# Optimization experiments

Hardware: AMD Instinct MI355X
Metric: run time of the kernel (lower is better)

Reference implementation:

```python
import jax, jax.numpy as jnp
import numpy as np

NUM_ATOMS = 50000
NUM_EDGES = 200000  # even: edges come in (fwd, rev) pairs
D_V, D_E, D_H = 133, 14, 256
DEPTH = 3


def setup_inputs() -> dict:
    key = jax.random.key(0)
    ks = jax.random.split(key, 12)
    half = NUM_EDGES // 2
    src = jax.random.randint(ks[0], (half,), 0, NUM_ATOMS)
    dst = jax.random.randint(ks[1], (half,), 0, NUM_ATOMS)
    v = jnp.concatenate([src, dst])
    w = jnp.concatenate([dst, src])
    edge_index = jnp.stack([v, w])  # [2, E]
    rev_edge_index = jnp.concatenate([jnp.arange(half) + half, jnp.arange(half)])

    def lin(k, out_d, in_d):
        return jax.random.normal(k, (out_d, in_d), jnp.float32) / np.sqrt(in_d)

    return {
        "V": jax.random.normal(ks[2], (NUM_ATOMS, D_V), jnp.float32),
        "E_feat": jax.random.normal(ks[3], (NUM_EDGES, D_E), jnp.float32),
        "edge_index": edge_index,
        "rev_edge_index": rev_edge_index,
        "Wi_atom": lin(ks[4], D_H, D_V),
        "Wi_bond": lin(ks[5], D_H, D_V + D_E),
        "Wh_atom": lin(ks[6], D_H, D_H),
        "Wh_bond": lin(ks[7], D_H, D_H),
        "Wf_atom": lin(ks[8], D_H, D_H),
        "Wf_bond": lin(ks[9], D_H, D_H),
        "Wo_atom": lin(ks[10], D_H, D_V + D_H),
    }


def _sum_and_max_into_atoms(H_e, w_idx, num_atoms):
    a_sum = jax.ops.segment_sum(H_e, w_idx, num_segments=num_atoms)
    a_max = jax.ops.segment_max(H_e, w_idx, num_segments=num_atoms)
    a_max = jnp.where(jnp.isfinite(a_max), a_max, 0.0)  # empty segments -> 0
    return a_sum, a_max


def _fuse(H, m, Wf):
    # Fusion(kind='mlp', residual=True), dropout=0:
    # residual update with a small MLP on the combined signal
    return H + jax.nn.relu((H + m) @ Wf.T)


def reference(V, E_feat, edge_index, rev_edge_index, Wi_atom, Wi_bond,
              Wh_atom, Wh_bond, Wf_atom, Wf_bond, Wo_atom):
    tau = jax.nn.relu
    num_atoms = V.shape[0]
    v = edge_index[0]
    w = edge_index[1]

    H_a = tau(V @ Wi_atom.T)                                        # [N, d_h]
    H_b = tau(jnp.concatenate([V[v], E_feat], axis=1) @ Wi_bond.T)  # [E, d_h]

    for _ in range(1, DEPTH):
        a_sum, a_max = _sum_and_max_into_atoms(H_b, w, num_atoms)
        gate = a_sum * a_max
        m_a = gate @ Wh_atom.T
        H_a = _fuse(H_a, m_a, Wf_atom)

        M_b = a_sum[v] - H_b[rev_edge_index]
        m_b = M_b @ Wh_bond.T
        H_b = _fuse(H_b, m_b, Wf_bond)

    a_sum, _ = _sum_and_max_into_atoms(H_b, w, num_atoms)
    H_atom = tau(jnp.concatenate([V, a_sum], axis=1) @ Wo_atom.T)   # [N, d_h]
    return H_atom
```

## Files before the change

kernel.cpp:

```cpp
#include <hip/hip_runtime.h>
#include <hip/hip_bf16.h>

#define NATOM 50000
#define NEDGE 200000
#define HALF  100000
#define DV    133
#define DE    14
#define DH    256
#define KVP   160
#define NBLK_SCAN ((NATOM + 255) / 256)

typedef __bf16  bf16x8 __attribute__((ext_vector_type(8)));
typedef __bf16  bf16x4 __attribute__((ext_vector_type(4)));
typedef float   f32x4  __attribute__((ext_vector_type(4)));

enum { EPI_RELU = 0, EPI_ADDBASE = 1, EPI_FUSE = 2, EPI_NONE = 3, EPI_RELUADD = 4 };
enum { AM_PLAIN = 0, AM_GATE = 1, AM_GDIFF = 2, AM_VF32 = 3, AM_XB = 4, AM_F32 = 5 };

__device__ __forceinline__ void gll16(const void* g, void* l) {
    __builtin_amdgcn_global_load_lds(
        (const __attribute__((address_space(1))) unsigned int*)g,
        (__attribute__((address_space(3))) unsigned int*)l, 16, 0, 0);
}
__device__ __forceinline__ void drain_barrier() {
    __builtin_amdgcn_s_waitcnt(0);
    __syncthreads();
}

struct GArgs {
    const __bf16* A; int lda;
    const float* asumf; const __bf16* amaxb;
    const __bf16* HbG; const int* vidx; const int* rev;
    const float* Vf; const float* Ef;
    const __bf16* W; int ldw;
    const __bf16* base; __bf16* C; float* Cf;
    int Mloc; int part0; int off0; int off1;
};

template<int AMODE, int EPI, int CLOC, int STF32, int KITERS>
__global__ __launch_bounds__(512, 2) void gemmk(GArgs g, int nblk) {
    __shared__ __bf16 Alds[4096];
    __shared__ __bf16 Blds[8192];
    const int tid  = threadIdx.x;
    const int lane = tid & 63, wv = tid >> 6;
    const int quad = lane >> 4, l16 = lane & 15;
    const int wr = (wv >> 2) * 64, wc = (wv & 3) * 64;
    const int lrow = lane >> 2, lu = lane & 3;

    for (int blk = blockIdx.x; blk < nblk; blk += gridDim.x) {
        const int gr0 = blk * 128;

        const int rs = tid >> 2, seg = tid & 3;
        const float *sp = nullptr; const __bf16 *hp = nullptr, *mp = nullptr;
        const float *vp = nullptr, *ep = nullptr;
        if (AMODE != AM_PLAIN) {
            int grs = gr0 + rs; if (grs > g.Mloc - 1) grs = g.Mloc - 1;
            const int maps = (grs < g.part0) ? g.off0 + grs : g.off1 + grs - g.part0;
            if (AMODE == AM_GATE)  { sp = g.asumf + (size_t)maps * DH; mp = g.amaxb + (size_t)maps * DH; }
            if (AMODE == AM_GDIFF) { sp = g.asumf + (size_t)g.vidx[maps] * DH; hp = g.HbG + (size_t)g.rev[maps] * DH; }
            if (AMODE == AM_F32)   { sp = g.asumf + (size_t)maps * DH; }
            if (AMODE == AM_VF32)  { vp = g.Vf + (size_t)maps * DV; }
            if (AMODE == AM_XB)    { vp = g.Vf + (size_t)g.vidx[maps] * DV; ep = g.Ef + (size_t)maps * DE; }
        }

        f32x4 acc[16];
#pragma unroll
        for (int i = 0; i < 16; ++i) acc[i] = (f32x4){0.f, 0.f, 0.f, 0.f};

        for (int kk = 0; kk < KITERS; ++kk) {
#pragma unroll
            for (int s = 0; s < 2; ++s) {
                int cl = (wv * 2 + s) * 16 + lrow;
                gll16(g.W + (size_t)cl * g.ldw + kk * 32 + lu * 8,
                      Blds + (wv * 2 + s) * 512);
            }
            if (AMODE == AM_PLAIN) {
                int r = wv * 16 + lrow;
                int gra = gr0 + r; if (gra > g.Mloc - 1) gra = g.Mloc - 1;
                gll16(g.A + (size_t)gra * g.lda + kk * 32 + lu * 8,
                      Alds + wv * 512);
            } else {
                bf16x8 o0;
                const int cb = kk * 32 + seg * 8;
                if (AMODE == AM_GATE || AMODE == AM_GDIFF || AMODE == AM_F32) {
                    f32x4 s0 = *(const f32x4*)(sp + cb);
                    f32x4 s1 = *(const f32x4*)(sp + cb + 4);
                    if (AMODE == AM_GATE) {
                        bf16x8 m0 = *(const bf16x8*)(mp + cb);
#pragma unroll
                        for (int j = 0; j < 4; ++j) {
                            o0[j]     = (__bf16)(s0[j] * (float)m0[j]);
                            o0[4 + j] = (__bf16)(s1[j] * (float)m0[4 + j]);
                        }
                    } else if (AMODE == AM_GDIFF) {
                        bf16x8 h0 = *(const bf16x8*)(hp + cb);
#pragma unroll
                        for (int j = 0; j < 4; ++j) {
                            o0[j]     = (__bf16)(s0[j] - (float)h0[j]);
                            o0[4 + j] = (__bf16)(s1[j] - (float)h0[4 + j]);
                        }
                    } else {
#pragma unroll
                        for (int j = 0; j < 4; ++j) {
                            o0[j]     = (__bf16)s0[j];
                            o0[4 + j] = (__bf16)s1[j];
                        }
                    }
                } else {
                    if (kk < 4) {
                        f32x4 x0, x1;
                        __builtin_memcpy(&x0, vp + cb, 16);
                        __builtin_memcpy(&x1, vp + cb + 4, 16);
#pragma unroll
                        for (int j = 0; j < 4; ++j) {
                            o0[j] = (__bf16)x0[j]; o0[4 + j] = (__bf16)x1[j];
                        }
                    } else {
#pragma unroll
                        for (int j = 0; j < 8; ++j) {
                            int c0 = cb + j;
                            float y0 = 0.f;
                            if (c0 < DV) y0 = vp[c0];
                            else if (AMODE == AM_XB && c0 < DV + DE) y0 = ep[c0 - DV];
                            o0[j] = (__bf16)y0;
                        }
                    }
                }
                *(bf16x8*)(Alds + rs * 32 + seg * 8) = o0;
            }
            drain_barrier();

            bf16x8 af[4], bfv[4];
#pragma unroll
            for (int m = 0; m < 4; ++m)
                af[m] = *(const bf16x8*)(Alds + (wr + m * 16 + l16) * 32 + quad * 8);
#pragma unroll
            for (int n = 0; n < 4; ++n)
                bfv[n] = *(const bf16x8*)(Blds + (wc + n * 16 + l16) * 32 + quad * 8);
#pragma unroll
            for (int m = 0; m < 4; ++m)
#pragma unroll
                for (int n = 0; n < 4; ++n)
                    acc[m * 4 + n] = __builtin_amdgcn_mfma_f32_16x16x32_bf16(
                        af[m], bfv[n], acc[m * 4 + n], 0, 0, 0);
            drain_barrier();
        }

#pragma unroll
        for (int m = 0; m < 4; ++m)
#pragma unroll
        for (int n = 0; n < 4; ++n)
#pragma unroll
        for (int r = 0; r < 4; ++r) {
            int gr = gr0 + wr + m * 16 + quad * 4 + r;
            if (gr < g.Mloc) {
                int mapped = (gr < g.part0) ? g.off0 + gr : g.off1 + gr - g.part0;
                int crow = CLOC ? gr : mapped;
                int col = wc + n * 16 + l16;
                size_t co = (size_t)crow * DH + col;
                float v = acc[m * 4 + n][r];
                float res;
                if (EPI == EPI_RELU)       res = v > 0.f ? v : 0.f;
                else if (EPI == EPI_NONE)  res = v;
                else {
                    float b = (float)g.base[(size_t)mapped * DH + col];
                    if (EPI == EPI_ADDBASE)      res = b + v;
                    else if (EPI == EPI_FUSE)    res = b + (v > 0.f ? v : 0.f);
                    else        { res = b + v; res = res > 0.f ? res : 0.f; }
                }
                if (STF32) g.Cf[co] = res;
                else       g.C[co]  = (__bf16)res;
            }
        }
    }
}

__global__ void count_deg(const int* __restrict__ widx, int* __restrict__ cnt) {
    int e = blockIdx.x * 256 + threadIdx.x;
    if (e < NEDGE) atomicAdd(&cnt[widx[e]], 1);
}

__global__ __launch_bounds__(256) void scan_p1(const int* __restrict__ cnt,
                                               int* __restrict__ rowptr,
                                               int* __restrict__ bsum) {
    __shared__ int sm[256];
    const int tid = threadIdx.x;
    const int i = blockIdx.x * 256 + tid;
    int v = (i < NATOM) ? cnt[i] : 0;
    sm[tid] = v;
    __syncthreads();
    for (int off = 1; off < 256; off <<= 1) {
        int t = (tid >= off) ? sm[tid - off] : 0;
        __syncthreads();
        sm[tid] += t;
        __syncthreads();
    }
    if (i < NATOM) rowptr[i] = sm[tid] - v;
    if (tid == 255) bsum[blockIdx.x] = sm[255];
}

__global__ __launch_bounds__(256) void scan_p2(int* __restrict__ bsum) {
    __shared__ int sm[256];
    const int tid = threadIdx.x;
    int v = (tid < NBLK_SCAN) ? bsum[tid] : 0;
    sm[tid] = v;
    __syncthreads();
    for (int off = 1; off < 256; off <<= 1) {
        int t = (tid >= off) ? sm[tid - off] : 0;
        __syncthreads();
        sm[tid] += t;
        __syncthreads();
    }
    if (tid < NBLK_SCAN) bsum[tid] = sm[tid] - v;
    if (tid == 255) bsum[NBLK_SCAN] = sm[255];
}

__global__ __launch_bounds__(256) void scan_p3(int* __restrict__ rowptr,
                                               int* __restrict__ cursor,
                                               const int* __restrict__ bsum) {
    const int i = blockIdx.x * 256 + threadIdx.x;
    if (i < NATOM) {
        int r = rowptr[i] + bsum[blockIdx.x];
        rowptr[i] = r;
        cursor[i] = r;
    }
    if (i == 0) rowptr[NATOM] = bsum[NBLK_SCAN];
}

__global__ void fill_csr(const int* __restrict__ widx, int* __restrict__ cursor,
                         int* __restrict__ eid) {
    int e = blockIdx.x * 256 + threadIdx.x;
    if (e >= NEDGE) return;
    int pos = atomicAdd(&cursor[widx[e]], 1);
    eid[pos] = e;
}

template<int WITHMAX>
__global__ __launch_bounds__(256) void seg_reduce(
    const __bf16* __restrict__ Hb, const int* __restrict__ rowptr,
    const int* __restrict__ eid,
    float* __restrict__ asum, __bf16* __restrict__ amaxb)
{
    int a = blockIdx.x * 4 + (threadIdx.x >> 6);
    if (a >= NATOM) return;
    const int lane = threadIdx.x & 63;
    const int beg = rowptr[a], end = rowptr[a + 1];
    float s0 = 0.f, s1 = 0.f, s2 = 0.f, s3 = 0.f;
    float m0 = 0.f, m1 = 0.f, m2 = 0.f, m3 = 0.f;
    for (int i = beg; i < end; ++i) {
        int e = eid[i];
        bf16x4 h = *(const bf16x4*)(Hb + (size_t)e * DH + lane * 4);
        float v0 = (float)h[0], v1 = (float)h[1], v2 = (float)h[2], v3 = (float)h[3];
        s0 += v0; s1 += v1; s2 += v2; s3 += v3;
        if (WITHMAX) {
            m0 = fmaxf(m0, v0); m1 = fmaxf(m1, v1);
            m2 = fmaxf(m2, v2); m3 = fmaxf(m3, v3);
        }
    }
    size_t o = (size_t)a * DH + lane * 4;
    *(f32x4*)(asum + o) = (f32x4){s0, s1, s2, s3};
    if (WITHMAX) {
        bf16x4 mv; mv[0] = (__bf16)m0; mv[1] = (__bf16)m1; mv[2] = (__bf16)m2; mv[3] = (__bf16)m3;
        *(bf16x4*)(amaxb + o) = mv;
    }
}

__global__ void pad_w2(const float* __restrict__ src, __bf16* __restrict__ dst,
                       int srcld, int coloff, int KS, int KD) {
    int i = blockIdx.x * 256 + threadIdx.x;
    if (i >= 256 * KD) return;
    int n = i / KD, c = i - n * KD;
    dst[i] = (c < KS) ? (__bf16)src[(size_t)n * srcld + coloff + c] : (__bf16)0.f;
}

static inline int cdiv(long a, long b) { return (int)((a + b - 1) / b); }
static inline int gsz2(int nblk) { return nblk < 2048 ? nblk : 2048; }

extern "C" void kernel_launch(void* const* d_in, const int* in_sizes, int n_in,
                              void* d_out, int out_size, void* d_ws, size_t ws_size,
                              hipStream_t stream) {
    const float* V    = (const float*)d_in[0];
    const float* Ef   = (const float*)d_in[1];
    const int*   ei   = (const int*)d_in[2];
    const int*   rev  = (const int*)d_in[3];
    const float* Wi_a = (const float*)d_in[4];
    const float* Wi_b = (const float*)d_in[5];
    const float* Wh_a = (const float*)d_in[6];
    const float* Wh_b = (const float*)d_in[7];
    const float* Wf_a = (const float*)d_in[8];
    const float* Wf_b = (const float*)d_in[9];
    const float* Wo   = (const float*)d_in[10];
    float* out = (float*)d_out;

    const int* vidx = ei;
    const int* widx = ei + NEDGE;

    char* ws = (char*)d_ws;
    __bf16* Hb    = (__bf16*)(ws + 0);
    __bf16* Ha    = (__bf16*)(ws + 102400000);
    char*   S     = ws + 128000000;
    float*  asum  = (float*)(ws + 192000000);
    __bf16* amaxb = (__bf16*)(S + 0);
    __bf16* Ta    = (__bf16*)(S + 25600000);
    __bf16* Tb    = (__bf16*)(S + 0);
    __bf16* T     = (__bf16*)(S + 25600000);
    __bf16* Wia   = (__bf16*)(ws + 243200000);
    __bf16* Wib   = (__bf16*)(ws + 243281920);
    __bf16* Wo1   = (__bf16*)(ws + 243363840);
    __bf16* Wo2   = (__bf16*)(ws + 243445760);
    __bf16* Wha   = (__bf16*)(ws + 243576832);
    __bf16* Whb   = (__bf16*)(ws + 243707904);
    __bf16* Wfa   = (__bf16*)(ws + 243838976);
    __bf16* Wfb   = (__bf16*)(ws + 243970048);
    int*  rowptr  = (int*)(ws + 244101120);
    int*  cursor  = (int*)(ws + 244301312);
    int*  eid     = (int*)(ws + 244501504);
    int*  bsum    = (int*)(ws + 128000000);
    (void)ws_size;

    hipMemsetAsync(cursor, 0, NATOM * sizeof(int), stream);
    count_deg<<<cdiv(NEDGE, 256), 256, 0, stream>>>(widx, cursor);
    scan_p1<<<NBLK_SCAN, 256, 0, stream>>>(cursor, rowptr, bsum);
    scan_p2<<<1, 256, 0, stream>>>(bsum);
    scan_p3<<<NBLK_SCAN, 256, 0, stream>>>(rowptr, cursor, bsum);
    fill_csr<<<cdiv(NEDGE, 256), 256, 0, stream>>>(widx, cursor, eid);

    pad_w2<<<cdiv(256 * KVP, 256), 256, 0, stream>>>(Wi_a, Wia, DV, 0, DV, KVP);
    pad_w2<<<cdiv(256 * KVP, 256), 256, 0, stream>>>(Wi_b, Wib, DV + DE, 0, DV + DE, KVP);
    pad_w2<<<cdiv(256 * KVP, 256), 256, 0, stream>>>(Wo, Wo1, DV + DH, 0, DV, KVP);
    pad_w2<<<cdiv(256 * DH, 256), 256, 0, stream>>>(Wo, Wo2, DV + DH, DV, DH, DH);
    pad_w2<<<cdiv(256 * DH, 256), 256, 0, stream>>>(Wh_a, Wha, DH, 0, DH, DH);
    pad_w2<<<cdiv(256 * DH, 256), 256, 0, stream>>>(Wh_b, Whb, DH, 0, DH, DH);
    pad_w2<<<cdiv(256 * DH, 256), 256, 0, stream>>>(Wf_a, Wfa, DH, 0, DH, DH);
    pad_w2<<<cdiv(256 * DH, 256), 256, 0, stream>>>(Wf_b, Wfb, DH, 0, DH, DH);

    GArgs ga{};
    ga.asumf = asum; ga.amaxb = amaxb; ga.HbG = Hb; ga.vidx = vidx; ga.rev = rev;
    ga.Vf = V; ga.Ef = Ef;

    {
        int nblk = cdiv(NATOM, 128);
        ga.W = Wia; ga.ldw = KVP; ga.C = Ha;
        ga.Mloc = NATOM; ga.part0 = NATOM; ga.off0 = 0; ga.off1 = 0;
        gemmk<AM_VF32, EPI_RELU, 0, 0, 5><<<gsz2(nblk), 512, 0, stream>>>(ga, nblk);
    }
    {
        int nblk = cdiv(NEDGE, 128);
        ga.W = Wib; ga.ldw = KVP; ga.C = Hb;
        ga.Mloc = NEDGE; ga.part0 = NEDGE; ga.off0 = 0; ga.off1 = 0;
        gemmk<AM_XB, EPI_RELU, 0, 0, 5><<<gsz2(nblk), 512, 0, stream>>>(ga, nblk);
    }

    for (int it = 0; it < 2; ++it) {
        seg_reduce<1><<<cdiv(NATOM, 4), 256, 0, stream>>>(Hb, rowptr, eid, asum, amaxb);

        {
            int nblk = cdiv(NATOM, 128);
            ga.W = Wha; ga.ldw = DH; ga.base = Ha; ga.C = Ta;
            ga.Mloc = NATOM; ga.part0 = NATOM; ga.off0 = 0; ga.off1 = 0;
            gemmk<AM_GATE, EPI_ADDBASE, 1, 0, 8><<<gsz2(nblk), 512, 0, stream>>>(ga, nblk);
            ga.A = Ta; ga.lda = DH; ga.W = Wfa; ga.base = Ha; ga.C = Ha;
            gemmk<AM_PLAIN, EPI_FUSE, 0, 0, 8><<<gsz2(nblk), 512, 0, stream>>>(ga, nblk);
        }

        for (int c = 0; c < 2; ++c) {
            int nblk = cdiv(HALF, 128);
            ga.W = Whb; ga.ldw = DH; ga.base = Hb; ga.C = Tb;
            ga.Mloc = HALF; ga.part0 = HALF / 2; ga.off0 = c * 50000; ga.off1 = HALF + c * 50000;
            gemmk<AM_GDIFF, EPI_ADDBASE, 1, 0, 8><<<gsz2(nblk), 512, 0, stream>>>(ga, nblk);
            ga.A = Tb; ga.lda = DH; ga.W = Wfb; ga.base = Hb; ga.C = Hb;
            gemmk<AM_PLAIN, EPI_FUSE, 0, 0, 8><<<gsz2(nblk), 512, 0, stream>>>(ga, nblk);
        }
    }

    seg_reduce<0><<<cdiv(NATOM, 4), 256, 0, stream>>>(Hb, rowptr, eid, asum, nullptr);
    {
        int nblk = cdiv(NATOM, 128);
        ga.Mloc = NATOM; ga.part0 = NATOM; ga.off0 = 0; ga.off1 = 0;
        ga.W = Wo1; ga.ldw = KVP; ga.C = T;
        gemmk<AM_VF32, EPI_NONE, 0, 0, 5><<<gsz2(nblk), 512, 0, stream>>>(ga, nblk);
        ga.W = Wo2; ga.ldw = DH; ga.base = T; ga.Cf = out;
        gemmk<AM_F32, EPI_RELUADD, 0, 1, 8><<<gsz2(nblk), 512, 0, stream>>>(ga, nblk);
    }
}
```

Measured before the change: 1.204 ms.

## Preload full A tile into LDS and double-buffer W tiles in GEMM

The GEMM used to load one 32-wide K slice of A and W per iteration, with two full barriers each time. Now all K slices of the gathered or converted A rows are staged into LDS in one pass before any compute. W tiles are double-buffered, and the next slice is prefetched while MFMAs run on the current one. This aims to raise memory-level parallelism and hide global load latency behind compute. The cost is much larger LDS use: 96KB for K=256, which likely stops two 512-thread blocks from sharing a CU and so lowers occupancy.

```diff
diff --git a/kernel.cpp b/kernel.cpp
--- a/kernel.cpp
+++ b/kernel.cpp
@@ -39,8 +39,8 @@
 
 template<int AMODE, int EPI, int CLOC, int STF32, int KITERS>
 __global__ __launch_bounds__(512, 2) void gemmk(GArgs g, int nblk) {
-    __shared__ __bf16 Alds[4096];
-    __shared__ __bf16 Blds[8192];
+    __shared__ __align__(16) __bf16 Alds[KITERS * 4096];
+    __shared__ __align__(16) __bf16 Blds[2 * 8192];
     const int tid  = threadIdx.x;
     const int lane = tid & 63, wv = tid >> 6;
     const int quad = lane >> 4, l16 = lane & 15;
@@ -63,23 +63,20 @@
             if (AMODE == AM_XB)    { vp = g.Vf + (size_t)g.vidx[maps] * DV; ep = g.Ef + (size_t)maps * DE; }
         }
 
-        f32x4 acc[16];
-#pragma unroll
-        for (int i = 0; i < 16; ++i) acc[i] = (f32x4){0.f, 0.f, 0.f, 0.f};
-
-        for (int kk = 0; kk < KITERS; ++kk) {
-#pragma unroll
-            for (int s = 0; s < 2; ++s) {
-                int cl = (wv * 2 + s) * 16 + lrow;
-                gll16(g.W + (size_t)cl * g.ldw + kk * 32 + lu * 8,
-                      Blds + (wv * 2 + s) * 512);
-            }
-            if (AMODE == AM_PLAIN) {
-                int r = wv * 16 + lrow;
-                int gra = gr0 + r; if (gra > g.Mloc - 1) gra = g.Mloc - 1;
+#pragma unroll
+        for (int s = 0; s < 2; ++s) {
+            int cl = (wv * 2 + s) * 16 + lrow;
+            gll16(g.W + (size_t)cl * g.ldw + lu * 8, Blds + (wv * 2 + s) * 512);
+        }
+        if (AMODE == AM_PLAIN) {
+            int gra = gr0 + wv * 16 + lrow; if (gra > g.Mloc - 1) gra = g.Mloc - 1;
+#pragma unroll
+            for (int kk = 0; kk < KITERS; ++kk)
                 gll16(g.A + (size_t)gra * g.lda + kk * 32 + lu * 8,
-                      Alds + wv * 512);
-            } else {
+                      Alds + kk * 4096 + wv * 512);
+        } else {
+#pragma unroll
+            for (int kk = 0; kk < KITERS; ++kk) {
                 bf16x8 o0;
                 const int cb = kk * 32 + seg * 8;
                 if (AMODE == AM_GATE || AMODE == AM_GDIFF || AMODE == AM_F32) {
@@ -126,17 +123,33 @@
                         }
                     }
                 }
-                *(bf16x8*)(Alds + rs * 32 + seg * 8) = o0;
+                *(bf16x8*)(Alds + kk * 4096 + rs * 32 + seg * 8) = o0;
             }
-            drain_barrier();
-
+        }
+        drain_barrier();
+
+        f32x4 acc[16];
+#pragma unroll
+        for (int i = 0; i < 16; ++i) acc[i] = (f32x4){0.f, 0.f, 0.f, 0.f};
+
+        for (int k = 0; k < KITERS; ++k) {
+            if (k + 1 < KITERS) {
+#pragma unroll
+                for (int s = 0; s < 2; ++s) {
+                    int cl = (wv * 2 + s) * 16 + lrow;
+                    gll16(g.W + (size_t)cl * g.ldw + (k + 1) * 32 + lu * 8,
+                          Blds + ((k + 1) & 1) * 8192 + (wv * 2 + s) * 512);
+                }
+            }
+            const __bf16* Ak = Alds + k * 4096;
+            const __bf16* Bb = Blds + (k & 1) * 8192;
             bf16x8 af[4], bfv[4];
 #pragma unroll
             for (int m = 0; m < 4; ++m)
-                af[m] = *(const bf16x8*)(Alds + (wr + m * 16 + l16) * 32 + quad * 8);
+                af[m] = *(const bf16x8*)(Ak + (wr + m * 16 + l16) * 32 + quad * 8);
 #pragma unroll
             for (int n = 0; n < 4; ++n)
-                bfv[n] = *(const bf16x8*)(Blds + (wc + n * 16 + l16) * 32 + quad * 8);
+                bfv[n] = *(const bf16x8*)(Bb + (wc + n * 16 + l16) * 32 + quad * 8);
 #pragma unroll
             for (int m = 0; m < 4; ++m)
 #pragma unroll
```

Result: slower. 1.326 ms (+10.1%).

## Fuse chained message/fusion GEMMs via LDS and load operands directly to registers

Applied to the files above, without the earlier changes.

Replaces the generic LDS-staged GEMM with two kernels. One is a direct-to-register GEMM for the input and output projections; the final Wo projection now runs as a single K-concatenated pass instead of two launches through an intermediate buffer. The other is a fused two-GEMM kernel that keeps the Wh result in swizzled LDS and feeds it straight into the Wf GEMM with the residual ReLU epilogue. For bonds, each block processes forward and reverse edge pairs together so that H_b[rev] is read from rows the same block updates, and a bf16 copy of a_sum is emitted for this path. This removes intermediate global round trips, extra launches and barriers, at the cost of uncoalesced per-lane global operand loads, repeated weight reads from cache, and slightly lower precision in the bond message.

```diff
diff --git a/kernel.cpp b/kernel.cpp
--- a/kernel.cpp
+++ b/kernel.cpp
@@ -14,163 +14,251 @@
 typedef __bf16  bf16x4 __attribute__((ext_vector_type(4)));
 typedef float   f32x4  __attribute__((ext_vector_type(4)));
 
-enum { EPI_RELU = 0, EPI_ADDBASE = 1, EPI_FUSE = 2, EPI_NONE = 3, EPI_RELUADD = 4 };
-enum { AM_PLAIN = 0, AM_GATE = 1, AM_GDIFF = 2, AM_VF32 = 3, AM_XB = 4, AM_F32 = 5 };
-
-__device__ __forceinline__ void gll16(const void* g, void* l) {
-    __builtin_amdgcn_global_load_lds(
-        (const __attribute__((address_space(1))) unsigned int*)g,
-        (__attribute__((address_space(3))) unsigned int*)l, 16, 0, 0);
-}
 __device__ __forceinline__ void drain_barrier() {
     __builtin_amdgcn_s_waitcnt(0);
     __syncthreads();
 }
 
-struct GArgs {
-    const __bf16* A; int lda;
-    const float* asumf; const __bf16* amaxb;
-    const __bf16* HbG; const int* vidx; const int* rev;
-    const float* Vf; const float* Ef;
-    const __bf16* W; int ldw;
-    const __bf16* base; __bf16* C; float* Cf;
-    int Mloc; int part0; int off0; int off1;
+
+struct DArgs {
+    const float* Vf; const float* Ef; const float* asumf;
+    const int* vidx;
+    const __bf16* W1; const __bf16* W2;
+    __bf16* C; float* Cf;
+    int M;
 };
 
-template<int AMODE, int EPI, int CLOC, int STF32, int KITERS>
-__global__ __launch_bounds__(512, 2) void gemmk(GArgs g, int nblk) {
-    __shared__ __bf16 Alds[4096];
-    __shared__ __bf16 Blds[8192];
-    const int tid  = threadIdx.x;
+template<int MODE, int KITERS>
+__global__ __launch_bounds__(512, 4) void dgemm(DArgs g) {
+    const int tid = threadIdx.x;
     const int lane = tid & 63, wv = tid >> 6;
     const int quad = lane >> 4, l16 = lane & 15;
     const int wr = (wv >> 2) * 64, wc = (wv & 3) * 64;
-    const int lrow = lane >> 2, lu = lane & 3;
-
-    for (int blk = blockIdx.x; blk < nblk; blk += gridDim.x) {
-        const int gr0 = blk * 128;
-
-        const int rs = tid >> 2, seg = tid & 3;
-        const float *sp = nullptr; const __bf16 *hp = nullptr, *mp = nullptr;
-        const float *vp = nullptr, *ep = nullptr;
-        if (AMODE != AM_PLAIN) {
-            int grs = gr0 + rs; if (grs > g.Mloc - 1) grs = g.Mloc - 1;
-            const int maps = (grs < g.part0) ? g.off0 + grs : g.off1 + grs - g.part0;
-            if (AMODE == AM_GATE)  { sp = g.asumf + (size_t)maps * DH; mp = g.amaxb + (size_t)maps * DH; }
-            if (AMODE == AM_GDIFF) { sp = g.asumf + (size_t)g.vidx[maps] * DH; hp = g.HbG + (size_t)g.rev[maps] * DH; }
-            if (AMODE == AM_F32)   { sp = g.asumf + (size_t)maps * DH; }
-            if (AMODE == AM_VF32)  { vp = g.Vf + (size_t)maps * DV; }
-            if (AMODE == AM_XB)    { vp = g.Vf + (size_t)g.vidx[maps] * DV; ep = g.Ef + (size_t)maps * DE; }
-        }
-
-        f32x4 acc[16];
-#pragma unroll
-        for (int i = 0; i < 16; ++i) acc[i] = (f32x4){0.f, 0.f, 0.f, 0.f};
-
-        for (int kk = 0; kk < KITERS; ++kk) {
-#pragma unroll
-            for (int s = 0; s < 2; ++s) {
-                int cl = (wv * 2 + s) * 16 + lrow;
-                gll16(g.W + (size_t)cl * g.ldw + kk * 32 + lu * 8,
-                      Blds + (wv * 2 + s) * 512);
-            }
-            if (AMODE == AM_PLAIN) {
-                int r = wv * 16 + lrow;
-                int gra = gr0 + r; if (gra > g.Mloc - 1) gra = g.Mloc - 1;
-                gll16(g.A + (size_t)gra * g.lda + kk * 32 + lu * 8,
-                      Alds + wv * 512);
-            } else {
-                bf16x8 o0;
-                const int cb = kk * 32 + seg * 8;
-                if (AMODE == AM_GATE || AMODE == AM_GDIFF || AMODE == AM_F32) {
-                    f32x4 s0 = *(const f32x4*)(sp + cb);
-                    f32x4 s1 = *(const f32x4*)(sp + cb + 4);
-                    if (AMODE == AM_GATE) {
-                        bf16x8 m0 = *(const bf16x8*)(mp + cb);
-#pragma unroll
-                        for (int j = 0; j < 4; ++j) {
-                            o0[j]     = (__bf16)(s0[j] * (float)m0[j]);
-                            o0[4 + j] = (__bf16)(s1[j] * (float)m0[4 + j]);
-                        }
-                    } else if (AMODE == AM_GDIFF) {
-                        bf16x8 h0 = *(const bf16x8*)(hp + cb);
-#pragma unroll
-                        for (int j = 0; j < 4; ++j) {
-                            o0[j]     = (__bf16)(s0[j] - (float)h0[j]);
-                            o0[4 + j] = (__bf16)(s1[j] - (float)h0[4 + j]);
-                        }
-                    } else {
-#pragma unroll
-                        for (int j = 0; j < 4; ++j) {
-                            o0[j]     = (__bf16)s0[j];
-                            o0[4 + j] = (__bf16)s1[j];
-                        }
+    const int gr0 = blockIdx.x * 128;
+
+    int vrow[4]; const float* epp[4];
+#pragma unroll
+    for (int m = 0; m < 4; ++m) {
+        int r = gr0 + wr + m * 16 + l16;
+        if (r > g.M - 1) r = g.M - 1;
+        vrow[m] = (MODE == 1) ? g.vidx[r] : r;
+        epp[m] = (MODE == 1) ? (g.Ef + (size_t)r * DE) : nullptr;
+    }
+
+    f32x4 acc[16];
+#pragma unroll
+    for (int i = 0; i < 16; ++i) acc[i] = (f32x4){0.f, 0.f, 0.f, 0.f};
+
+#pragma unroll
+    for (int kk = 0; kk < KITERS; ++kk) {
+        bf16x8 af[4];
+#pragma unroll
+        for (int m = 0; m < 4; ++m) {
+            const int cb = kk * 32 + quad * 8;
+            if (MODE != 2 || kk < 5) {
+                const float* vp = g.Vf + (size_t)vrow[m] * DV;
+                if (kk < 4) {
+                    f32x4 x0, x1;
+                    __builtin_memcpy(&x0, vp + cb, 16);
+                    __builtin_memcpy(&x1, vp + cb + 4, 16);
+#pragma unroll
+                    for (int j = 0; j < 4; ++j) {
+                        af[m][j] = (__bf16)x0[j]; af[m][4 + j] = (__bf16)x1[j];
                     }
                 } else {
-                    if (kk < 4) {
-                        f32x4 x0, x1;
-                        __builtin_memcpy(&x0, vp + cb, 16);
-                        __builtin_memcpy(&x1, vp + cb + 4, 16);
-#pragma unroll
-                        for (int j = 0; j < 4; ++j) {
-                            o0[j] = (__bf16)x0[j]; o0[4 + j] = (__bf16)x1[j];
-                        }
-                    } else {
-#pragma unroll
-                        for (int j = 0; j < 8; ++j) {
-                            int c0 = cb + j;
-                            float y0 = 0.f;
-                            if (c0 < DV) y0 = vp[c0];
-                            else if (AMODE == AM_XB && c0 < DV + DE) y0 = ep[c0 - DV];
-                            o0[j] = (__bf16)y0;
-                        }
+#pragma unroll
+                    for (int j = 0; j < 8; ++j) {
+                        int c = cb + j; float y = 0.f;
+                        if (c < DV) y = vp[c];
+                        else if (MODE == 1 && c < DV + DE) y = epp[m][c - DV];
+                        af[m][j] = (__bf16)y;
                     }
                 }
-                *(bf16x8*)(Alds + rs * 32 + seg * 8) = o0;
+            } else {
+                const float* sp = g.asumf + (size_t)vrow[m] * DH + (kk - 5) * 32 + quad * 8;
+                f32x4 s0 = *(const f32x4*)sp, s1 = *(const f32x4*)(sp + 4);
+#pragma unroll
+                for (int j = 0; j < 4; ++j) {
+                    af[m][j] = (__bf16)s0[j]; af[m][4 + j] = (__bf16)s1[j];
+                }
             }
-            drain_barrier();
-
-            bf16x8 af[4], bfv[4];
-#pragma unroll
-            for (int m = 0; m < 4; ++m)
-                af[m] = *(const bf16x8*)(Alds + (wr + m * 16 + l16) * 32 + quad * 8);
+        }
+        bf16x8 bfv[4];
+#pragma unroll
+        for (int n = 0; n < 4; ++n) {
+            int col = wc + n * 16 + l16;
+            const __bf16* wp;
+            if (MODE == 2 && kk >= 5) wp = g.W2 + (size_t)col * DH  + (kk - 5) * 32 + quad * 8;
+            else                      wp = g.W1 + (size_t)col * KVP + kk * 32 + quad * 8;
+            bfv[n] = *(const bf16x8*)wp;
+        }
+#pragma unroll
+        for (int m = 0; m < 4; ++m)
 #pragma unroll
             for (int n = 0; n < 4; ++n)
-                bfv[n] = *(const bf16x8*)(Blds + (wc + n * 16 + l16) * 32 + quad * 8);
-#pragma unroll
-            for (int m = 0; m < 4; ++m)
-#pragma unroll
-                for (int n = 0; n < 4; ++n)
-                    acc[m * 4 + n] = __builtin_amdgcn_mfma_f32_16x16x32_bf16(
-                        af[m], bfv[n], acc[m * 4 + n], 0, 0, 0);
-            drain_barrier();
-        }
-
+                acc[m * 4 + n] = __builtin_amdgcn_mfma_f32_16x16x32_bf16(
+                    af[m], bfv[n], acc[m * 4 + n], 0, 0, 0);
+    }
+
+#pragma unroll
+    for (int m = 0; m < 4; ++m)
+#pragma unroll
+    for (int n = 0; n < 4; ++n)
+#pragma unroll
+    for (int r = 0; r < 4; ++r) {
+        int gr = gr0 + wr + m * 16 + quad * 4 + r;
+        if (gr < g.M) {
+            int col = wc + n * 16 + l16;
+            float v = acc[m * 4 + n][r];
+            v = v > 0.f ? v : 0.f;
+            if (MODE == 2) g.Cf[(size_t)gr * DH + col] = v;
+            else           g.C [(size_t)gr * DH + col] = (__bf16)v;
+        }
+    }
+}
+
+struct FArgs {
+    const float* asumf; const __bf16* asumb; const __bf16* amaxb;
+    const int* vidx;
+    const __bf16* W1; const __bf16* W2;
+    __bf16* H;
+    int M;
+};
+
+__device__ __forceinline__ int tswz(int row, int byteInRow) {
+    return ((row << 9) + byteInRow) ^ ((row & 7) << 4);
+}
+
+template<int BOND>
+__global__ __launch_bounds__(512, 4) void fgemm(FArgs g) {
+    __shared__ __bf16 Tlds[32768];
+    const int tid = threadIdx.x;
+    const int lane = tid & 63, wv = tid >> 6;
+    const int quad = lane >> 4, l16 = lane & 15;
+    const int wr = (wv >> 2) * 64, wc = (wv & 3) * 64;
+
+    int grow[4], hrow[4];
+#pragma unroll
+    for (int m = 0; m < 4; ++m) {
+        int lr = wr + m * 16 + l16;
+        if (BOND) {
+            int sl = blockIdx.x * 64 + (lr & 63);
+            if (sl > g.M - 1) sl = g.M - 1;
+            int gA = (lr < 64) ? sl : g.M + sl;
+            hrow[m] = (lr < 64) ? g.M + sl : sl;
+            grow[m] = g.vidx[gA];
+        } else {
+            int r = blockIdx.x * 128 + lr;
+            if (r > g.M - 1) r = g.M - 1;
+            grow[m] = r; hrow[m] = r;
+        }
+    }
+
+    f32x4 acc[16];
+#pragma unroll
+    for (int i = 0; i < 16; ++i) acc[i] = (f32x4){0.f, 0.f, 0.f, 0.f};
+
+#pragma unroll
+    for (int kk = 0; kk < 8; ++kk) {
+        const int cb = kk * 32 + quad * 8;
+        bf16x8 af[4];
+#pragma unroll
+        for (int m = 0; m < 4; ++m) {
+            if (BOND) {
+                bf16x8 a = *(const bf16x8*)(g.asumb + (size_t)grow[m] * DH + cb);
+                bf16x8 h = *(const bf16x8*)(g.H     + (size_t)hrow[m] * DH + cb);
+#pragma unroll
+                for (int j = 0; j < 8; ++j)
+                    af[m][j] = (__bf16)((float)a[j] - (float)h[j]);
+            } else {
+                const float* s = g.asumf + (size_t)grow[m] * DH + cb;
+                f32x4 s0 = *(const f32x4*)s, s1 = *(const f32x4*)(s + 4);
+                bf16x8 mx = *(const bf16x8*)(g.amaxb + (size_t)grow[m] * DH + cb);
+#pragma unroll
+                for (int j = 0; j < 4; ++j) {
+                    af[m][j]     = (__bf16)(s0[j] * (float)mx[j]);
+                    af[m][4 + j] = (__bf16)(s1[j] * (float)mx[4 + j]);
+                }
+            }
+        }
+        bf16x8 bfv[4];
+#pragma unroll
+        for (int n = 0; n < 4; ++n)
+            bfv[n] = *(const bf16x8*)(g.W1 + (size_t)(wc + n * 16 + l16) * DH + cb);
 #pragma unroll
         for (int m = 0; m < 4; ++m)
 #pragma unroll
+            for (int n = 0; n < 4; ++n)
+                acc[m * 4 + n] = __builtin_amdgcn_mfma_f32_16x16x32_bf16(
+                    af[m], bfv[n], acc[m * 4 + n], 0, 0, 0);
+    }
+
+#pragma unroll
+    for (int m = 0; m < 4; ++m)
+#pragma unroll
+    for (int n = 0; n < 4; ++n)
+#pragma unroll
+    for (int r = 0; r < 4; ++r) {
+        int lr = wr + m * 16 + quad * 4 + r;
+        int gOut;
+        if (BOND) {
+            int sl = blockIdx.x * 64 + (lr & 63);
+            if (sl > g.M - 1) sl = g.M - 1;
+            gOut = (lr < 64) ? sl : g.M + sl;
+        } else {
+            gOut = blockIdx.x * 128 + lr;
+            if (gOut > g.M - 1) gOut = g.M - 1;
+        }
+        int col = wc + n * 16 + l16;
+        float b = (float)g.H[(size_t)gOut * DH + col];
+        *(__bf16*)((char*)Tlds + tswz(lr, col * 2)) = (__bf16)(b + acc[m * 4 + n][r]);
+    }
+    drain_barrier();
+
+#pragma unroll
+    for (int i = 0; i < 16; ++i) acc[i] = (f32x4){0.f, 0.f, 0.f, 0.f};
+#pragma unroll
+    for (int kk = 0; kk < 8; ++kk) {
+        bf16x8 af[4], bfv[4];
+#pragma unroll
+        for (int m = 0; m < 4; ++m) {
+            int lr = wr + m * 16 + l16;
+            af[m] = *(const bf16x8*)((const char*)Tlds + tswz(lr, kk * 64 + quad * 16));
+        }
+#pragma unroll
         for (int n = 0; n < 4; ++n)
-#pragma unroll
-        for (int r = 0; r < 4; ++r) {
-            int gr = gr0 + wr + m * 16 + quad * 4 + r;
-            if (gr < g.Mloc) {
-                int mapped = (gr < g.part0) ? g.off0 + gr : g.off1 + gr - g.part0;
-                int crow = CLOC ? gr : mapped;
-                int col = wc + n * 16 + l16;
-                size_t co = (size_t)crow * DH + col;
-                float v = acc[m * 4 + n][r];
-                float res;
-                if (EPI == EPI_RELU)       res = v > 0.f ? v : 0.f;
-                else if (EPI == EPI_NONE)  res = v;
-                else {
-                    float b = (float)g.base[(size_t)mapped * DH + col];
-                    if (EPI == EPI_ADDBASE)      res = b + v;
-                    else if (EPI == EPI_FUSE)    res = b + (v > 0.f ? v : 0.f);
-                    else        { res = b + v; res = res > 0.f ? res : 0.f; }
-                }
-                if (STF32) g.Cf[co] = res;
-                else       g.C[co]  = (__bf16)res;
-            }
+            bfv[n] = *(const bf16x8*)(g.W2 + (size_t)(wc + n * 16 + l16) * DH + kk * 32 + quad * 8);
+#pragma unroll
+        for (int m = 0; m < 4; ++m)
+#pragma unroll
+            for (int n = 0; n < 4; ++n)
+                acc[m * 4 + n] = __builtin_amdgcn_mfma_f32_16x16x32_bf16(
+                    af[m], bfv[n], acc[m * 4 + n], 0, 0, 0);
+    }
+
+#pragma unroll
+    for (int m = 0; m < 4; ++m)
+#pragma unroll
+    for (int n = 0; n < 4; ++n)
+#pragma unroll
+    for (int r = 0; r < 4; ++r) {
+        int lr = wr + m * 16 + quad * 4 + r;
+        bool ok; int gOut;
+        if (BOND) {
+            int sl = blockIdx.x * 64 + (lr & 63);
+            ok = sl < g.M;
+            gOut = (lr < 64) ? sl : g.M + sl;
+        } else {
+            gOut = blockIdx.x * 128 + lr;
+            ok = gOut < g.M;
+        }
+        if (ok) {
+            int col = wc + n * 16 + l16;
+            size_t o = (size_t)gOut * DH + col;
+            float b = (float)g.H[o];
+            float v = acc[m * 4 + n][r];
+            v = v > 0.f ? v : 0.f;
+            g.H[o] = (__bf16)(b + v);
         }
     }
 }
@@ -239,7 +327,8 @@
 __global__ __launch_bounds__(256) void seg_reduce(
     const __bf16* __restrict__ Hb, const int* __restrict__ rowptr,
     const int* __restrict__ eid,
-    float* __restrict__ asum, __bf16* __restrict__ amaxb)
+    float* __restrict__ asum, __bf16* __restrict__ asumb,
+    __bf16* __restrict__ amaxb)
 {
     int a = blockIdx.x * 4 + (threadIdx.x >> 6);
     if (a >= NATOM) return;
@@ -260,6 +349,8 @@
     size_t o = (size_t)a * DH + lane * 4;
     *(f32x4*)(asum + o) = (f32x4){s0, s1, s2, s3};
     if (WITHMAX) {
+        bf16x4 sv; sv[0] = (__bf16)s0; sv[1] = (__bf16)s1; sv[2] = (__bf16)s2; sv[3] = (__bf16)s3;
+        *(bf16x4*)(asumb + o) = sv;
         bf16x4 mv; mv[0] = (__bf16)m0; mv[1] = (__bf16)m1; mv[2] = (__bf16)m2; mv[3] = (__bf16)m3;
         *(bf16x4*)(amaxb + o) = mv;
     }
@@ -274,7 +365,6 @@
 }
 
 static inline int cdiv(long a, long b) { return (int)((a + b - 1) / b); }
-static inline int gsz2(int nblk) { return nblk < 2048 ? nblk : 2048; }
 
 extern "C" void kernel_launch(void* const* d_in, const int* in_sizes, int n_in,
                               void* d_out, int out_size, void* d_ws, size_t ws_size,
@@ -291,6 +381,7 @@
     const float* Wf_b = (const float*)d_in[9];
     const float* Wo   = (const float*)d_in[10];
     float* out = (float*)d_out;
+    (void)rev;
 
     const int* vidx = ei;
     const int* widx = ei + NEDGE;
@@ -298,24 +389,21 @@
     char* ws = (char*)d_ws;
     __bf16* Hb    = (__bf16*)(ws + 0);
     __bf16* Ha    = (__bf16*)(ws + 102400000);
-    char*   S     = ws + 128000000;
-    float*  asum  = (float*)(ws + 192000000);
-    __bf16* amaxb = (__bf16*)(S + 0);
-    __bf16* Ta    = (__bf16*)(S + 25600000);
-    __bf16* Tb    = (__bf16*)(S + 0);
-    __bf16* T     = (__bf16*)(S + 25600000);
-    __bf16* Wia   = (__bf16*)(ws + 243200000);
-    __bf16* Wib   = (__bf16*)(ws + 243281920);
-    __bf16* Wo1   = (__bf16*)(ws + 243363840);
-    __bf16* Wo2   = (__bf16*)(ws + 243445760);
-    __bf16* Wha   = (__bf16*)(ws + 243576832);
-    __bf16* Whb   = (__bf16*)(ws + 243707904);
-    __bf16* Wfa   = (__bf16*)(ws + 243838976);
-    __bf16* Wfb   = (__bf16*)(ws + 243970048);
-    int*  rowptr  = (int*)(ws + 244101120);
-    int*  cursor  = (int*)(ws + 244301312);
-    int*  eid     = (int*)(ws + 244501504);
-    int*  bsum    = (int*)(ws + 128000000);
+    float*  asum  = (float*) (ws + 128000000);
+    __bf16* asumb = (__bf16*)(ws + 179200000);
+    __bf16* amaxb = (__bf16*)(ws + 204800000);
+    __bf16* Wia   = (__bf16*)(ws + 230400000);
+    __bf16* Wib   = (__bf16*)(ws + 230481920);
+    __bf16* Wo1   = (__bf16*)(ws + 230563840);
+    __bf16* Wo2   = (__bf16*)(ws + 230645760);
+    __bf16* Wha   = (__bf16*)(ws + 230776832);
+    __bf16* Whb   = (__bf16*)(ws + 230907904);
+    __bf16* Wfa   = (__bf16*)(ws + 231038976);
+    __bf16* Wfb   = (__bf16*)(ws + 231170048);
+    int*  rowptr  = (int*)(ws + 231301120);
+    int*  cursor  = (int*)(ws + 231501312);
+    int*  eid     = (int*)(ws + 231701504);
+    int*  bsum    = (int*)(ws + 232501504);
     (void)ws_size;
 
     hipMemsetAsync(cursor, 0, NATOM * sizeof(int), stream);
@@ -334,52 +422,32 @@
     pad_w2<<<cdiv(256 * DH, 256), 256, 0, stream>>>(Wf_a, Wfa, DH, 0, DH, DH);
     pad_w2<<<cdiv(256 * DH, 256), 256, 0, stream>>>(Wf_b, Wfb, DH, 0, DH, DH);
 
-    GArgs ga{};
-    ga.asumf = asum; ga.amaxb = amaxb; ga.HbG = Hb; ga.vidx = vidx; ga.rev = rev;
-    ga.Vf = V; ga.Ef = Ef;
-
     {
-        int nblk = cdiv(NATOM, 128);
-        ga.W = Wia; ga.ldw = KVP; ga.C = Ha;
-        ga.Mloc = NATOM; ga.part0 = NATOM; ga.off0 = 0; ga.off1 = 0;
-        gemmk<AM_VF32, EPI_RELU, 0, 0, 5><<<gsz2(nblk), 512, 0, stream>>>(ga, nblk);
+        DArgs d{}; d.Vf = V; d.W1 = Wia; d.C = Ha; d.M = NATOM;
+        dgemm<0, 5><<<cdiv(NATOM, 128), 512, 0, stream>>>(d);
     }
     {
-        int nblk = cdiv(NEDGE, 128);
-        ga.W = Wib; ga.ldw = KVP; ga.C = Hb;
-        ga.Mloc = NEDGE; ga.part0 = NEDGE; ga.off0 = 0; ga.off1 = 0;
-        gemmk<AM_XB, EPI_RELU, 0, 0, 5><<<gsz2(nblk), 512, 0, stream>>>(ga, nblk);
+        DArgs d{}; d.Vf = V; d.Ef = Ef; d.vidx = vidx; d.W1 = Wib; d.C = Hb; d.M = NEDGE;
+        dgemm<1, 5><<<cdiv(NEDGE, 128), 512, 0, stream>>>(d);
     }
 
     for (int it = 0; it < 2; ++it) {
-        seg_reduce<1><<<cdiv(NATOM, 4), 256, 0, stream>>>(Hb, rowptr, eid, asum, amaxb);
-
+        seg_reduce<1><<<cdiv(NATOM, 4), 256, 0, stream>>>(Hb, rowptr, eid, asum, asumb, amaxb);
         {
-            int nblk = cdiv(NATOM, 128);
-            ga.W = Wha; ga.ldw = DH; ga.base = Ha; ga.C = Ta;
-            ga.Mloc = NATOM; ga.part0 = NATOM; ga.off0 = 0; ga.off1 = 0;
-            gemmk<AM_GATE, EPI_ADDBASE, 1, 0, 8><<<gsz2(nblk), 512, 0, stream>>>(ga, nblk);
-            ga.A = Ta; ga.lda = DH; ga.W = Wfa; ga.base = Ha; ga.C = Ha;
-            gemmk<AM_PLAIN, EPI_FUSE, 0, 0, 8><<<gsz2(nblk), 512, 0, stream>>>(ga, nblk);
-        }
-
-        for (int c = 0; c < 2; ++c) {
-            int nblk = cdiv(HALF, 128);
-            ga.W = Whb; ga.ldw = DH; ga.base = Hb; ga.C = Tb;
-            ga.Mloc = HALF; ga.part0 = HALF / 2; ga.off0 = c * 50000; ga.off1 = HALF + c * 50000;
-            gemmk<AM_GDIFF, EPI_ADDBASE, 1, 0, 8><<<gsz2(nblk), 512, 0, stream>>>(ga, nblk);
-            ga.A = Tb; ga.lda = DH; ga.W = Wfb; ga.base = Hb; ga.C = Hb;
-            gemmk<AM_PLAIN, EPI_FUSE, 0, 0, 8><<<gsz2(nblk), 512, 0, stream>>>(ga, nblk);
-        }
-    }
-
-    seg_reduce<0><<<cdiv(NATOM, 4), 256, 0, stream>>>(Hb, rowptr, eid, asum, nullptr);
+            FArgs f{}; f.asumf = asum; f.amaxb = amaxb;
+            f.W1 = Wha; f.W2 = Wfa; f.H = Ha; f.M = NATOM;
+            fgemm<0><<<cdiv(NATOM, 128), 512, 0, stream>>>(f);
+        }
+        {
+            FArgs f{}; f.asumb = asumb; f.vidx = vidx;
+            f.W1 = Whb; f.W2 = Wfb; f.H = Hb; f.M = HALF;
+            fgemm<1><<<cdiv(HALF, 64), 512, 0, stream>>>(f);
+        }
+    }
+
+    seg_reduce<0><<<cdiv(NATOM, 4), 256, 0, stream>>>(Hb, rowptr, eid, asum, nullptr, nullptr);
     {
-        int nblk = cdiv(NATOM, 128);
-        ga.Mloc = NATOM; ga.part0 = NATOM; ga.off0 = 0; ga.off1 = 0;
-        ga.W = Wo1; ga.ldw = KVP; ga.C = T;
-        gemmk<AM_VF32, EPI_NONE, 0, 0, 5><<<gsz2(nblk), 512, 0, stream>>>(ga, nblk);
-        ga.W = Wo2; ga.ldw = DH; ga.base = T; ga.Cf = out;
-        gemmk<AM_F32, EPI_RELUADD, 0, 1, 8><<<gsz2(nblk), 512, 0, stream>>>(ga, nblk);
-    }
-}
+        DArgs d{}; d.Vf = V; d.asumf = asum; d.W1 = Wo1; d.W2 = Wo2; d.Cf = out; d.M = NATOM;
+        dgemm<2, 13><<<cdiv(NATOM, 128), 512, 0, stream>>>(d);
+    }
+}
```

Result: slower. 1.366 ms (+13.4%).
